# Kernel optimization log

Measured on AMD Instinct MI355X. Metric: run time of the kernel, lower is better.

## Reference

```python
import jax, jax.numpy as jnp
import numpy as np

MARGIN = 0.1
PERM_SEED = 42  # fixed stand-in for torch.randperm per row


def setup_inputs() -> dict:
    key = jax.random.key(0)
    k1, k2, k3 = jax.random.split(key, 3)
    n, d, f = 32768, 1000, 300
    inputs = jax.random.normal(k1, (n, f), dtype=jnp.float32)
    Y = jax.random.normal(k2, (d, f), dtype=jnp.float32)
    y_idxs = jax.random.randint(k3, (n,), 0, d)
    return {"inputs": inputs, "Y": Y, "y_idxs": y_idxs}


def reference(inputs, Y, y_idxs):
    # inputs: [n, f], Y: [d, f] class semantic embeddings, y_idxs: [n]
    n, d = inputs.shape[0], Y.shape[0]

    # All dot products at once: S[i, j] = Y[j] . inputs[i]
    S = inputs @ Y.T  # [n, d]

    # One random class permutation per row (torch.randperm(d) per sample)
    perm_keys = jax.random.split(jax.random.key(PERM_SEED), n)
    perms = jax.vmap(lambda k: jax.random.permutation(k, d))(perm_keys)  # [n, d]

    ap = S[jnp.arange(n), y_idxs]                 # [n]   anchor-positive dots
    an = jnp.take_along_axis(S, perms, axis=1)    # [n, d] anchor-negative dots in perm order

    valid = perms != y_idxs[:, None]              # skip j == y
    # early-break condition at each permutation slot
    cond = valid & ((ap[:, None] - an) > MARGIN)
    c = cond.astype(jnp.int32)
    excl_cum = jnp.cumsum(c, axis=1) - c          # exclusive cumsum of break events
    # include every valid slot up to AND including the first breaking slot
    include = valid & (excl_cum == 0)             # [n, d]

    # MarginRankingLoss with target=1: mean(max(0, margin + an - ap))
    per_pair = jnp.maximum(0.0, MARGIN + an - ap[:, None])
    total = jnp.sum(jnp.where(include, per_pair, 0.0))
    count = jnp.maximum(jnp.sum(include), 1).astype(jnp.float32)
    return total / count
```

## Files before the change

### kernel.cpp

```cpp
#include <hip/hip_runtime.h>
#include <stdint.h>

#define N_ROWS 32768
#define D_CLS  1000
#define D_PAD  1024
#define F_DIM  300
#define F_PAD  320
#define MARGIN 0.1f

#define BM     128
#define BN     128
#define BK     64
#define GTHR   512
#define LDTA   328
#define LDTB   72

#define M_PB   32
#define NTHR   512
#define NT_PW  8
#define MT_PB  2
#define LDA    328
#define SROW   34

#define NPART  32

typedef short short8 __attribute__((ext_vector_type(8)));
typedef float f32x4  __attribute__((ext_vector_type(4)));

__device__ __forceinline__ uint32_t rotl32(uint32_t x, int r) {
  return (x << r) | (x >> (32 - r));
}

__device__ __forceinline__ void threefry2x32(uint32_t k0, uint32_t k1,
                                             uint32_t x0, uint32_t x1,
                                             uint32_t& o0, uint32_t& o1) {
  uint32_t k2 = k0 ^ k1 ^ 0x1BD11BDAu;
  x0 += k0; x1 += k1;
#define TF_R(r) { x0 += x1; x1 = rotl32(x1, (r)); x1 ^= x0; }
  TF_R(13) TF_R(15) TF_R(26) TF_R(6)
  x0 += k1; x1 += k2 + 1u;
  TF_R(17) TF_R(29) TF_R(16) TF_R(24)
  x0 += k2; x1 += k0 + 2u;
  TF_R(13) TF_R(15) TF_R(26) TF_R(6)
  x0 += k0; x1 += k1 + 3u;
  TF_R(17) TF_R(29) TF_R(16) TF_R(24)
  x0 += k1; x1 += k2 + 4u;
  TF_R(13) TF_R(15) TF_R(26) TF_R(6)
  x0 += k2; x1 += k0 + 5u;
#undef TF_R
  o0 = x0; o1 = x1;
}

struct TFSched {
  uint32_t k0, k1, k2, k2p1, k0p2, k1p3, k2p4, k0p5;
};
__device__ __forceinline__ TFSched tf_make(uint32_t k0, uint32_t k1) {
  TFSched s;
  s.k0 = k0; s.k1 = k1;
  s.k2 = k0 ^ k1 ^ 0x1BD11BDAu;
  s.k2p1 = s.k2 + 1u; s.k0p2 = k0 + 2u; s.k1p3 = k1 + 3u;
  s.k2p4 = s.k2 + 4u; s.k0p5 = k0 + 5u;
  return s;
}
__device__ __forceinline__ uint32_t tf_hash(const TFSched& s, uint32_t c) {
  uint32_t x0 = s.k0, x1 = c + s.k1;
#define TFH(r) { x0 += x1; x1 = __builtin_amdgcn_alignbit(x1, x1, 32 - (r)); x1 ^= x0; }
  TFH(13) TFH(15) TFH(26) TFH(6)
  x0 += s.k1; x1 += s.k2p1;
  TFH(17) TFH(29) TFH(16) TFH(24)
  x0 += s.k2; x1 += s.k0p2;
  TFH(13) TFH(15) TFH(26) TFH(6)
  x0 += s.k0; x1 += s.k1p3;
  TFH(17) TFH(29) TFH(16) TFH(24)
  x0 += s.k1; x1 += s.k2p4;
  TFH(13) TFH(15) TFH(26) TFH(6)
  x0 += s.k2; x1 += s.k0p5;
#undef TFH
  return x0 ^ x1;
}

__device__ __forceinline__ uint16_t f2bf(float f) {
  uint32_t u = __builtin_bit_cast(uint32_t, f);
  return (uint16_t)((u + 0x7FFFu + ((u >> 16) & 1u)) >> 16);
}
__device__ __forceinline__ float bf2f(uint16_t v) {
  return __builtin_bit_cast(float, (uint32_t)v << 16);
}
__device__ __forceinline__ float bf2f_lo(uint32_t v) {
  return __builtin_bit_cast(float, v << 16);
}
__device__ __forceinline__ float bf2f_hi(uint32_t v) {
  return __builtin_bit_cast(float, v & 0xFFFF0000u);
}

__global__ void prep(const float* __restrict__ Y, uint16_t* __restrict__ Ybf,
                     uint32_t* __restrict__ subk) {
  int i = blockIdx.x * 256 + threadIdx.x;
  if (i < D_PAD * F_PAD) {
    int j = i / F_PAD;
    int k = i - j * F_PAD;
    float v = (j < D_CLS && k < F_DIM) ? Y[j * F_DIM + k] : 0.f;
    Ybf[i] = f2bf(v);
  }
  if (i < N_ROWS) {
    uint32_t r1, r2, s1, s2;
    threefry2x32(0u, 42u, 0u, (uint32_t)i, r1, r2);
    threefry2x32(r1, r2, 0u, 1u, s1, s2);
    subk[2 * i]     = s1;
    subk[2 * i + 1] = s2;
  }
}

template<int FUSED>
__launch_bounds__(GTHR, 1)
__global__ void gemm_core(const float* __restrict__ inputs,
                          const uint16_t* __restrict__ Ybf,
                          uint32_t* __restrict__ Spair,
                          uint32_t* __restrict__ keyP,
                          const uint32_t* __restrict__ subk,
                          const int* __restrict__ yidx,
                          float* __restrict__ rowSum,
                          int* __restrict__ rowCnt) {
  __shared__ __align__(16) uint16_t A_lds[BM * LDTA];
  __shared__ __align__(16) uint16_t B_lds[2][BN * LDTB];

  const int t    = threadIdx.x;
  const int wave = t >> 6;
  const int lane = t & 63;
  const int l15  = lane & 15;
  const int g    = lane >> 4;
  const int wm   = wave >> 1;
  const int wn   = wave & 1;
  const int r0   = blockIdx.x * BM;

  for (int i = t; i < BM * (F_DIM / 4); i += GTHR) {
    int r  = i / 75;
    int c4 = i - r * 75;
    float4 v = *(const float4*)(inputs + (size_t)(r0 + r) * F_DIM + c4 * 4);
    ushort4 o;
    o.x = f2bf(v.x); o.y = f2bf(v.y); o.z = f2bf(v.z); o.w = f2bf(v.w);
    *(ushort4*)&A_lds[r * LDTA + c4 * 4] = o;
  }
  for (int i = t; i < BM * 7; i += GTHR) {
    int r = i / 7, p = i - r * 7;
    *(ushort4*)&A_lds[r * LDTA + 300 + p * 4] = (ushort4){0, 0, 0, 0};
  }

  const int brow = t >> 3, bkof = t & 7;
  short8 bv[2];
  auto LOADB = [&](int tile) {
    const int c0 = (tile / 5) * BN;
    const int k0 = (tile % 5) * BK;
#pragma unroll
    for (int j = 0; j < 2; ++j)
      bv[j] = *(const short8*)(Ybf + (size_t)(c0 + j * 64 + brow) * F_PAD + k0 + bkof * 8);
  };
  auto WRITEB = [&](int buf) {
#pragma unroll
    for (int j = 0; j < 2; ++j)
      *(short8*)&B_lds[buf][(j * 64 + brow) * LDTB + bkof * 8] = bv[j];
  };

  f32x4 acc[2][4];
#pragma unroll
  for (int mt = 0; mt < 2; ++mt)
#pragma unroll
    for (int nt = 0; nt < 4; ++nt) acc[mt][nt] = (f32x4){0.f, 0.f, 0.f, 0.f};

  LOADB(0);
  __syncthreads();
  WRITEB(0);
  __syncthreads();

  const int NT = 8 * 5;
#pragma unroll 1
  for (int tile = 0; tile < NT; ++tile) {
    const int kt = tile % 5;
    if (tile < NT - 1) LOADB(tile + 1);

    if (FUSED && tile < 32) {
#pragma unroll
      for (int mm = 0; mm < 2; ++mm) {
        const int m = 2 * tile + mm;
        const size_t rpg = (size_t)(r0 >> 1) + m;
        const int rA = r0 + 2 * m;
        const TFSched sA = tf_make(subk[2 * rA],     subk[2 * rA + 1]);
        const TFSched sB = tf_make(subk[2 * rA + 2], subk[2 * rA + 3]);
#pragma unroll
        for (int half = 0; half < 2; ++half) {
          const uint32_t c = (uint32_t)(t + 512 * half);
          uint32_t kA = tf_hash(sA, c);
          uint32_t kB = tf_hash(sB, c);
          keyP[rpg * D_PAD + c] = (kA >> 16) | (kB & 0xFFFF0000u);
        }
      }
    }

    const uint16_t* Bc = B_lds[tile & 1];
#pragma unroll
    for (int ks = 0; ks < 2; ++ks) {
      short8 a[2], b[4];
#pragma unroll
      for (int mt = 0; mt < 2; ++mt)
        a[mt] = *(const short8*)&A_lds[(wm * 32 + mt * 16 + l15) * LDTA + kt * BK + ks * 32 + g * 8];
#pragma unroll
      for (int nt = 0; nt < 4; ++nt)
        b[nt] = *(const short8*)&Bc[(wn * 64 + nt * 16 + l15) * LDTB + ks * 32 + g * 8];
#pragma unroll
      for (int mt = 0; mt < 2; ++mt)
#pragma unroll
        for (int nt = 0; nt < 4; ++nt)
          acc[mt][nt] = __builtin_amdgcn_mfma_f32_16x16x32_bf16(a[mt], b[nt], acc[mt][nt], 0, 0, 0);
    }
    if (kt == 4) {
      const int c0 = (tile / 5) * BN;
#pragma unroll
      for (int mt = 0; mt < 2; ++mt)
#pragma unroll
        for (int nt = 0; nt < 4; ++nt) {
          const int col = c0 + wn * 64 + nt * 16 + l15;
#pragma unroll
          for (int p = 0; p < 2; ++p) {
            uint32_t lo = f2bf(acc[mt][nt][2 * p]);
            uint32_t hi = f2bf(acc[mt][nt][2 * p + 1]);
            size_t rp = (size_t)(r0 >> 1) + wm * 16 + mt * 8 + g * 2 + p;
            Spair[rp * D_PAD + col] = (hi << 16) | lo;
          }
          acc[mt][nt] = (f32x4){0.f, 0.f, 0.f, 0.f};
        }
    }
    if (tile < NT - 1) {
      WRITEB((tile + 1) & 1);
      __syncthreads();
    }
  }

  if (FUSED) {
    __syncthreads();
#pragma unroll 1
    for (int j = 0; j < 8; ++j) {
      const int rp_loc = wave * 8 + j;
      const size_t rpg = (size_t)(r0 >> 1) + rp_loc;
      const int rA = r0 + 2 * rp_loc;
      const int yA = yidx[rA], yB = yidx[rA + 1];
      const uint32_t* Sp = Spair + rpg * D_PAD;
      const uint32_t* Kp = keyP  + rpg * D_PAD;
      const float apA = bf2f_lo(Sp[yA]);
      const float apB = bf2f_hi(Sp[yB]);

      uint32_t an[16], kk[16];
#pragma unroll
      for (int q4 = 0; q4 < 4; ++q4) {
        uint4 v = *(const uint4*)(Sp + q4 * 256 + lane * 4);
        an[4 * q4 + 0] = v.x; an[4 * q4 + 1] = v.y;
        an[4 * q4 + 2] = v.z; an[4 * q4 + 3] = v.w;
        uint4 w = *(const uint4*)(Kp + q4 * 256 + lane * 4);
        kk[4 * q4 + 0] = w.x; kk[4 * q4 + 1] = w.y;
        kk[4 * q4 + 2] = w.z; kk[4 * q4 + 3] = w.w;
      }

      uint32_t mnA = 0xFFFFu, mnB = 0xFFFFu;
#pragma unroll
      for (int q = 0; q < 16; ++q) {
        const int c = (q >> 2) * 256 + lane * 4 + (q & 3);
        const uint32_t kA = kk[q] & 0xFFFFu, kB = kk[q] >> 16;
        const float anA = bf2f_lo(an[q]), anB = bf2f_hi(an[q]);
        if ((c < D_CLS) && (c != yA) && (apA - anA) > MARGIN) mnA = (kA < mnA) ? kA : mnA;
        if ((c < D_CLS) && (c != yB) && (apB - anB) > MARGIN) mnB = (kB < mnB) ? kB : mnB;
      }
#pragma unroll
      for (int off = 1; off < 64; off <<= 1) {
        uint32_t oA = __shfl_xor(mnA, off, 64);
        uint32_t oB = __shfl_xor(mnB, off, 64);
        mnA = (oA < mnA) ? oA : mnA;
        mnB = (oB < mnB) ? oB : mnB;
      }

      float smA = 0.f, smB = 0.f; int ctA = 0, ctB = 0;
#pragma unroll
      for (int q = 0; q < 16; ++q) {
        const int c = (q >> 2) * 256 + lane * 4 + (q & 3);
        const uint32_t kA = kk[q] & 0xFFFFu, kB = kk[q] >> 16;
        const float anA = bf2f_lo(an[q]), anB = bf2f_hi(an[q]);
        if ((c < D_CLS) && (c != yA) && kA < mnA) { smA += MARGIN + anA - apA; ctA += 1; }
        if ((c < D_CLS) && (c != yB) && kB < mnB) { smB += MARGIN + anB - apB; ctB += 1; }
      }
#pragma unroll
      for (int off = 1; off < 64; off <<= 1) {
        smA += __shfl_xor(smA, off, 64);
        smB += __shfl_xor(smB, off, 64);
        ctA += __shfl_xor(ctA, off, 64);
        ctB += __shfl_xor(ctB, off, 64);
      }
      if (lane == 0) {
        rowSum[rA]     = smA;  rowCnt[rA]     = ctA + (mnA != 0xFFFFu ? 1 : 0);
        rowSum[rA + 1] = smB;  rowCnt[rA + 1] = ctB + (mnB != 0xFFFFu ? 1 : 0);
      }
    }
  }
}

__launch_bounds__(256, 2)
__global__ void hash_loss(const uint32_t* __restrict__ Spair,
                          const uint32_t* __restrict__ subk,
                          const int* __restrict__ yidx,
                          float* __restrict__ rowSum,
                          int* __restrict__ rowCnt) {
  const int lane = threadIdx.x & 63;
  const int wave = threadIdx.x >> 6;
  const int rp   = blockIdx.x * 4 + wave;
  const int rA   = 2 * rp;
  const int rB   = 2 * rp + 1;

  const int yA = yidx[rA], yB = yidx[rB];
  const TFSched sA = tf_make(subk[2 * rA], subk[2 * rA + 1]);
  const TFSched sB = tf_make(subk[2 * rB], subk[2 * rB + 1]);

  const uint32_t* Sp = Spair + (size_t)rp * D_PAD;
  const float apA = bf2f_lo(Sp[yA]);
  const float apB = bf2f_hi(Sp[yB]);

  uint32_t an[16];
#pragma unroll
  for (int j = 0; j < 4; ++j) {
    uint4 v = *(const uint4*)(Sp + j * 256 + lane * 4);
    an[4 * j + 0] = v.x; an[4 * j + 1] = v.y;
    an[4 * j + 2] = v.z; an[4 * j + 3] = v.w;
  }

  uint32_t skAB[16];
  uint32_t pkA = 0xFFFFFFFFu, pkB = 0xFFFFFFFFu;
#pragma unroll
  for (int q = 0; q < 16; ++q) {
    const int c = (q >> 2) * 256 + lane * 4 + (q & 3);
    uint32_t kA = tf_hash(sA, (uint32_t)c);
    uint32_t kB = tf_hash(sB, (uint32_t)c);
    skAB[q] = (kA >> 16) | (kB & 0xFFFF0000u);
    float anA = bf2f_lo(an[q]);
    float anB = bf2f_hi(an[q]);
    if ((c < D_CLS) && (c != yA) && (apA - anA) > MARGIN) {
      pkA = (kA < pkA) ? kA : pkA;
    }
    if ((c < D_CLS) && (c != yB) && (apB - anB) > MARGIN) {
      pkB = (kB < pkB) ? kB : pkB;
    }
  }
#pragma unroll
  for (int off = 1; off < 64; off <<= 1) {
    uint32_t oA = __shfl_xor(pkA, off, 64);
    uint32_t oB = __shfl_xor(pkB, off, 64);
    pkA = (oA < pkA) ? oA : pkA;
    pkB = (oB < pkB) ? oB : pkB;
  }
  const uint32_t pA16 = pkA >> 16;
  const uint32_t pB16 = pkB >> 16;

  float smA = 0.f, smB = 0.f; int ctA = 0, ctB = 0;
#pragma unroll
  for (int q = 0; q < 16; ++q) {
    const int c = (q >> 2) * 256 + lane * 4 + (q & 3);
    float anA = bf2f_lo(an[q]);
    float anB = bf2f_hi(an[q]);
    if ((c < D_CLS) && (c != yA) && (skAB[q] & 0xFFFFu) < pA16) {
      smA += MARGIN + anA - apA; ctA += 1;
    }
    if ((c < D_CLS) && (c != yB) && (skAB[q] >> 16) < pB16) {
      smB += MARGIN + anB - apB; ctB += 1;
    }
  }
#pragma unroll
  for (int off = 1; off < 64; off <<= 1) {
    smA += __shfl_xor(smA, off, 64);
    smB += __shfl_xor(smB, off, 64);
    ctA += __shfl_xor(ctA, off, 64);
    ctB += __shfl_xor(ctB, off, 64);
  }
  if (lane == 0) {
    rowSum[rA] = smA;
    rowCnt[rA] = ctA + (pkA != 0xFFFFFFFFu ? 1 : 0);
    rowSum[rB] = smB;
    rowCnt[rB] = ctB + (pkB != 0xFFFFFFFFu ? 1 : 0);
  }
}

__launch_bounds__(NTHR, 4)
__global__ void triplet_fused(const float* __restrict__ inputs,
                              const uint16_t* __restrict__ Ybf,
                              const int* __restrict__ yidx,
                              float* __restrict__ rowSum,
                              int* __restrict__ rowCnt) {
  __shared__ __align__(16) uint16_t SH[D_PAD * SROW];
  __shared__ int      y_sh[M_PB];
  __shared__ uint32_t subk_sh[M_PB][2];

  const int t    = threadIdx.x;
  const int wave = t >> 6;
  const int lane = t & 63;
  const int l15  = lane & 15;
  const int g    = lane >> 4;
  const int row0 = blockIdx.x * M_PB;
  const int colbase = wave * (NT_PW * 16);

  if (t < M_PB) {
    y_sh[t] = yidx[row0 + t];
    uint32_t r1, r2, s1, s2;
    threefry2x32(0u, 42u, 0u, (uint32_t)(row0 + t), r1, r2);
    threefry2x32(r1, r2, 0u, 1u, s1, s2);
    subk_sh[t][0] = s1; subk_sh[t][1] = s2;
  }

  uint16_t* A_fl = SH;
  for (int i = t; i < M_PB * (F_DIM / 4); i += NTHR) {
    int r  = i / 75;
    int c4 = i - r * 75;
    float4 v = *(const float4*)(inputs + (size_t)(row0 + r) * F_DIM + c4 * 4);
    ushort4 o;
    o.x = f2bf(v.x); o.y = f2bf(v.y); o.z = f2bf(v.z); o.w = f2bf(v.w);
    *(ushort4*)&A_fl[r * LDA + c4 * 4] = o;
  }
  for (int i = t; i < M_PB * 5; i += NTHR) {
    int r = i / 5, p = i - r * 5;
    *(ushort4*)&A_fl[r * LDA + 300 + p * 4] = (ushort4){0, 0, 0, 0};
  }
  __syncthreads();

  f32x4 acc[MT_PB][NT_PW];
#pragma unroll
  for (int mt = 0; mt < MT_PB; ++mt)
#pragma unroll
    for (int nt = 0; nt < NT_PW; ++nt) acc[mt][nt] = (f32x4){0.f, 0.f, 0.f, 0.f};

  const uint16_t* gB[NT_PW];
#pragma unroll
  for (int nt = 0; nt < NT_PW; ++nt) {
    int j = colbase + nt * 16 + l15;
    gB[nt] = Ybf + (size_t)j * F_PAD + (g << 3);
  }
  const uint16_t* aBase = &A_fl[l15 * LDA + (g << 3)];

#pragma unroll 2
  for (int ks = 0; ks < F_PAD / 32; ++ks) {
    short8 b[NT_PW], a[MT_PB];
#pragma unroll
    for (int nt = 0; nt < NT_PW; ++nt)
      b[nt] = *(const short8*)(gB[nt] + ks * 32);
#pragma unroll
    for (int mt = 0; mt < MT_PB; ++mt)
      a[mt] = *(const short8*)(aBase + mt * 16 * LDA + ks * 32);
#pragma unroll
    for (int mt = 0; mt < MT_PB; ++mt)
#pragma unroll
      for (int nt = 0; nt < NT_PW; ++nt)
        acc[mt][nt] = __builtin_amdgcn_mfma_f32_16x16x32_bf16(a[mt], b[nt], acc[mt][nt], 0, 0, 0);
  }

  __syncthreads();

#pragma unroll
  for (int mt = 0; mt < MT_PB; ++mt)
#pragma unroll
    for (int nt = 0; nt < NT_PW; ++nt) {
      int col = colbase + nt * 16 + l15;
#pragma unroll
      for (int p = 0; p < 2; ++p) {
        uint32_t lo = f2bf(acc[mt][nt][2 * p]);
        uint32_t hi = f2bf(acc[mt][nt][2 * p + 1]);
        *(uint32_t*)&SH[col * SROW + mt * 16 + (g << 2) + 2 * p] = (hi << 16) | lo;
      }
    }
  __syncthreads();

#pragma unroll
  for (int pr = 0; pr < 2; ++pr) {
    const int rA = wave * 4 + pr * 2;
    const int rB = rA + 1;
    const int yA = y_sh[rA], yB = y_sh[rB];
    const uint32_t a1 = subk_sh[rA][0], a2 = subk_sh[rA][1];
    const uint32_t b1 = subk_sh[rB][0], b2 = subk_sh[rB][1];
    const float apA = bf2f(SH[yA * SROW + rA]);
    const float apB = bf2f(SH[yB * SROW + rB]);

    uint32_t skA[16], skB[16];
    uint32_t pkA = 0xFFFFFFFFu, pkB = 0xFFFFFFFFu;
#pragma unroll
    for (int q = 0; q < 16; ++q) {
      const int c = q * 64 + lane;
      uint32_t xA, yAo, xB, yBo;
      threefry2x32(a1, a2, 0u, (uint32_t)c, xA, yAo);
      threefry2x32(b1, b2, 0u, (uint32_t)c, xB, yBo);
      skA[q] = xA ^ yAo;
      skB[q] = xB ^ yBo;
      float anA = bf2f(SH[c * SROW + rA]);
      float anB = bf2f(SH[c * SROW + rB]);
      if ((c < D_CLS) && (c != yA) && (apA - anA) > MARGIN) {
        pkA = (skA[q] < pkA) ? skA[q] : pkA;
      }
      if ((c < D_CLS) && (c != yB) && (apB - anB) > MARGIN) {
        pkB = (skB[q] < pkB) ? skB[q] : pkB;
      }
    }
#pragma unroll
    for (int off = 1; off < 64; off <<= 1) {
      uint32_t oA = __shfl_xor(pkA, off, 64);
      uint32_t oB = __shfl_xor(pkB, off, 64);
      pkA = (oA < pkA) ? oA : pkA;
      pkB = (oB < pkB) ? oB : pkB;
    }
    float smA = 0.f, smB = 0.f; int ctA = 0, ctB = 0;
#pragma unroll
    for (int q = 0; q < 16; ++q) {
      const int c = q * 64 + lane;
      float anA = bf2f(SH[c * SROW + rA]);
      float anB = bf2f(SH[c * SROW + rB]);
      if ((c < D_CLS) && (c != yA) && skA[q] < pkA) { smA += MARGIN + anA - apA; ctA += 1; }
      if ((c < D_CLS) && (c != yB) && skB[q] < pkB) { smB += MARGIN + anB - apB; ctB += 1; }
    }
#pragma unroll
    for (int off = 1; off < 64; off <<= 1) {
      smA += __shfl_xor(smA, off, 64);
      smB += __shfl_xor(smB, off, 64);
      ctA += __shfl_xor(ctA, off, 64);
      ctB += __shfl_xor(ctB, off, 64);
    }
    if (lane == 0) {
      rowSum[row0 + rA] = smA;
      rowCnt[row0 + rA] = ctA + (pkA != 0xFFFFFFFFu ? 1 : 0);
      rowSum[row0 + rB] = smB;
      rowCnt[row0 + rB] = ctB + (pkB != 0xFFFFFFFFu ? 1 : 0);
    }
  }
}

__global__ void reduce_part(const float* __restrict__ rowSum,
                            const int* __restrict__ rowCnt,
                            float* __restrict__ pS, int* __restrict__ pC) {
  __shared__ float ss[4];
  __shared__ int   sc[4];
  const int base = blockIdx.x * (N_ROWS / NPART);
  float s = 0.f; int c = 0;
  for (int i = threadIdx.x; i < N_ROWS / NPART; i += 256) {
    s += rowSum[base + i];
    c += rowCnt[base + i];
  }
#pragma unroll
  for (int off = 32; off > 0; off >>= 1) {
    s += __shfl_down(s, (unsigned)off, 64);
    c += __shfl_down(c, (unsigned)off, 64);
  }
  int wid = threadIdx.x >> 6, lane = threadIdx.x & 63;
  if (lane == 0) { ss[wid] = s; sc[wid] = c; }
  __syncthreads();
  if (threadIdx.x == 0) {
    pS[blockIdx.x] = ss[0] + ss[1] + ss[2] + ss[3];
    pC[blockIdx.x] = sc[0] + sc[1] + sc[2] + sc[3];
  }
}

__global__ void reduce_final(const float* __restrict__ pS,
                             const int* __restrict__ pC,
                             float* __restrict__ out) {
  const int lane = threadIdx.x;
  float s = (lane < NPART) ? pS[lane] : 0.f;
  int   c = (lane < NPART) ? pC[lane] : 0;
#pragma unroll
  for (int off = 32; off > 0; off >>= 1) {
    s += __shfl_down(s, (unsigned)off, 64);
    c += __shfl_down(c, (unsigned)off, 64);
  }
  if (lane == 0) out[0] = s / (float)(c < 1 ? 1 : c);
}

extern "C" void kernel_launch(void* const* d_in, const int* in_sizes, int n_in,
                              void* d_out, int out_size, void* d_ws, size_t ws_size,
                              hipStream_t stream) {
  const float* inputs = (const float*)d_in[0];
  const float* Y      = (const float*)d_in[1];
  const int*   yidx   = (const int*)d_in[2];
  float* out = (float*)d_out;

  char* ws = (char*)d_ws;
  size_t off = 0;
  uint16_t* Ybf    = (uint16_t*)(ws + off); off += (size_t)D_PAD * F_PAD * 2;
  float*    rowSum = (float*)(ws + off);    off += (size_t)N_ROWS * 4;
  int*      rowCnt = (int*)(ws + off);      off += (size_t)N_ROWS * 4;
  uint32_t* subk   = (uint32_t*)(ws + off); off += (size_t)N_ROWS * 8;
  float*    pS     = (float*)(ws + off);    off += (size_t)NPART * 4;
  int*      pC     = (int*)(ws + off);      off += (size_t)NPART * 4;
  off = (off + 255) & ~(size_t)255;
  uint32_t* Spair  = (uint32_t*)(ws + off); off += (size_t)(N_ROWS / 2) * D_PAD * 4;
  const size_t need_mid = off;
  off = (off + 255) & ~(size_t)255;
  uint32_t* keyP   = (uint32_t*)(ws + off); off += (size_t)(N_ROWS / 2) * D_PAD * 4;
  const size_t need_full = off;

  hipLaunchKernelGGL(prep, dim3((D_PAD * F_PAD + 255) / 256), dim3(256),
                     0, stream, Y, Ybf, subk);
  if (ws_size >= need_full) {
    gemm_core<1><<<dim3(N_ROWS / BM), dim3(GTHR), 0, stream>>>(
        inputs, Ybf, Spair, keyP, subk, yidx, rowSum, rowCnt);
  } else if (ws_size >= need_mid) {
    gemm_core<0><<<dim3(N_ROWS / BM), dim3(GTHR), 0, stream>>>(
        inputs, Ybf, Spair, (uint32_t*)nullptr, subk, yidx, rowSum, rowCnt);
    hipLaunchKernelGGL(hash_loss, dim3(N_ROWS / 8), dim3(256),
                       0, stream, Spair, subk, yidx, rowSum, rowCnt);
  } else {
    hipLaunchKernelGGL(triplet_fused, dim3(N_ROWS / M_PB), dim3(NTHR),
                       0, stream, inputs, Ybf, yidx, rowSum, rowCnt);
  }
  hipLaunchKernelGGL(reduce_part, dim3(NPART), dim3(256), 0, stream,
                     rowSum, rowCnt, pS, pC);
  hipLaunchKernelGGL(reduce_final, dim3(1), dim3(64), 0, stream, pS, pC, out);
}
```

Before: 138.0 us.

## Warp-specialize GEMM with dedicated hash waves and split loss into separate kernel

The fused GEMM kernel is replaced by a 1024-thread block in which 8 waves do the MFMA GEMM while 8 extra waves compute the threefry permutation keys concurrently, writing them with vectorized 16-byte stores. The per-row loss evaluation moves out of the GEMM tail into a separate lightweight kernel. This is meant to overlap the hash ALU work with matrix math and to stop the loss tail from serializing inside the GEMM block. In exchange it adds a kernel launch, a re-read of Spair and keyP from memory, and a larger block that may reduce occupancy or register headroom.

After: 129.5 us. 1.07x faster.

```diff
diff --git a/kernel.cpp b/kernel.cpp
--- a/kernel.cpp
+++ b/kernel.cpp
@@ -12,6 +12,7 @@
 #define BN     128
 #define BK     64
 #define GTHR   512
+#define KGTHR  1024
 #define LDTA   328
 #define LDTB   72
 
@@ -111,16 +112,199 @@
   }
 }
 
-template<int FUSED>
+__launch_bounds__(KGTHR, 4)
+__global__ void gemm_kg(const float* __restrict__ inputs,
+                        const uint16_t* __restrict__ Ybf,
+                        uint32_t* __restrict__ Spair,
+                        uint32_t* __restrict__ keyP,
+                        const uint32_t* __restrict__ subk) {
+  __shared__ __align__(16) uint16_t A_lds[BM * LDTA];
+  __shared__ __align__(16) uint16_t B_lds[2][BN * LDTB];
+
+  const int t    = threadIdx.x;
+  const int wave = t >> 6;
+  const int lane = t & 63;
+  const int l15  = lane & 15;
+  const int g    = lane >> 4;
+  const bool isg = wave < 8;
+  const int wm   = wave >> 1;
+  const int wn   = wave & 1;
+  const int kw   = wave - 8;
+  const int r0   = blockIdx.x * BM;
+
+  for (int i = t; i < BM * (F_DIM / 4); i += KGTHR) {
+    int r  = i / 75;
+    int c4 = i - r * 75;
+    float4 v = *(const float4*)(inputs + (size_t)(r0 + r) * F_DIM + c4 * 4);
+    ushort4 o;
+    o.x = f2bf(v.x); o.y = f2bf(v.y); o.z = f2bf(v.z); o.w = f2bf(v.w);
+    *(ushort4*)&A_lds[r * LDTA + c4 * 4] = o;
+  }
+  for (int i = t; i < BM * 7; i += KGTHR) {
+    int r = i / 7, p = i - r * 7;
+    *(ushort4*)&A_lds[r * LDTA + 300 + p * 4] = (ushort4){0, 0, 0, 0};
+  }
+
+  const int brow = t >> 3, bkof = t & 7;
+  short8 bv[2];
+  auto LOADB = [&](int tile) {
+    const int c0 = (tile / 5) * BN;
+    const int k0 = (tile % 5) * BK;
+#pragma unroll
+    for (int j = 0; j < 2; ++j)
+      bv[j] = *(const short8*)(Ybf + (size_t)(c0 + j * 64 + brow) * F_PAD + k0 + bkof * 8);
+  };
+  auto WRITEB = [&](int buf) {
+#pragma unroll
+    for (int j = 0; j < 2; ++j)
+      *(short8*)&B_lds[buf][(j * 64 + brow) * LDTB + bkof * 8] = bv[j];
+  };
+
+  f32x4 acc[2][4];
+#pragma unroll
+  for (int mt = 0; mt < 2; ++mt)
+#pragma unroll
+    for (int nt = 0; nt < 4; ++nt) acc[mt][nt] = (f32x4){0.f, 0.f, 0.f, 0.f};
+
+  if (isg) LOADB(0);
+  __syncthreads();
+  if (isg) WRITEB(0);
+  __syncthreads();
+
+  const int NT = 8 * 5;
+#pragma unroll 1
+  for (int tile = 0; tile < NT; ++tile) {
+    if (isg) {
+      const int kt = tile % 5;
+      if (tile < NT - 1) LOADB(tile + 1);
+      const uint16_t* Bc = B_lds[tile & 1];
+#pragma unroll
+      for (int ks = 0; ks < 2; ++ks) {
+        short8 a[2], b[4];
+#pragma unroll
+        for (int mt = 0; mt < 2; ++mt)
+          a[mt] = *(const short8*)&A_lds[(wm * 32 + mt * 16 + l15) * LDTA + kt * BK + ks * 32 + g * 8];
+#pragma unroll
+        for (int nt = 0; nt < 4; ++nt)
+          b[nt] = *(const short8*)&Bc[(wn * 64 + nt * 16 + l15) * LDTB + ks * 32 + g * 8];
+#pragma unroll
+        for (int mt = 0; mt < 2; ++mt)
+#pragma unroll
+          for (int nt = 0; nt < 4; ++nt)
+            acc[mt][nt] = __builtin_amdgcn_mfma_f32_16x16x32_bf16(a[mt], b[nt], acc[mt][nt], 0, 0, 0);
+      }
+      if (kt == 4) {
+        const int c0 = (tile / 5) * BN;
+#pragma unroll
+        for (int mt = 0; mt < 2; ++mt)
+#pragma unroll
+          for (int nt = 0; nt < 4; ++nt) {
+            const int col = c0 + wn * 64 + nt * 16 + l15;
+#pragma unroll
+            for (int p = 0; p < 2; ++p) {
+              uint32_t lo = f2bf(acc[mt][nt][2 * p]);
+              uint32_t hi = f2bf(acc[mt][nt][2 * p + 1]);
+              size_t rp = (size_t)(r0 >> 1) + wm * 16 + mt * 8 + g * 2 + p;
+              Spair[rp * D_PAD + col] = (hi << 16) | lo;
+            }
+            acc[mt][nt] = (f32x4){0.f, 0.f, 0.f, 0.f};
+          }
+      }
+      if (tile < NT - 1) WRITEB((tile + 1) & 1);
+    } else if (tile < 32) {
+      const int rp_loc = kw * 8 + (tile >> 2);
+      const size_t rpg = (size_t)(r0 >> 1) + rp_loc;
+      const int rA = r0 + 2 * rp_loc;
+      const uint4 sk4 = *(const uint4*)(subk + 2 * rA);
+      const TFSched sA = tf_make(sk4.x, sk4.y);
+      const TFSched sB = tf_make(sk4.z, sk4.w);
+      const uint32_t c0 = (uint32_t)((tile & 3) * 256 + 4 * lane);
+      uint4 ov;
+      uint32_t o[4];
+#pragma unroll
+      for (int j = 0; j < 4; ++j) {
+        uint32_t kA = tf_hash(sA, c0 + (uint32_t)j);
+        uint32_t kB = tf_hash(sB, c0 + (uint32_t)j);
+        o[j] = (kA >> 16) | (kB & 0xFFFF0000u);
+      }
+      ov.x = o[0]; ov.y = o[1]; ov.z = o[2]; ov.w = o[3];
+      *(uint4*)(keyP + (rpg << 10) + c0) = ov;
+    }
+    if (tile < NT - 1) __syncthreads();
+  }
+}
+
+__launch_bounds__(256, 4)
+__global__ void loss_light(const uint32_t* __restrict__ Spair,
+                           const uint32_t* __restrict__ keyP,
+                           const int* __restrict__ yidx,
+                           float* __restrict__ rowSum,
+                           int* __restrict__ rowCnt) {
+  const int lane = threadIdx.x & 63;
+  const int wave = threadIdx.x >> 6;
+  const int rp   = blockIdx.x * 4 + wave;
+  const int rA   = 2 * rp;
+  const int rB   = rA + 1;
+  const int yA = yidx[rA], yB = yidx[rB];
+  const uint32_t* Sp = Spair + (size_t)rp * D_PAD;
+  const uint32_t* Kp = keyP  + (size_t)rp * D_PAD;
+  const float apA = bf2f_lo(Sp[yA]);
+  const float apB = bf2f_hi(Sp[yB]);
+
+  uint32_t an[16], kk[16];
+#pragma unroll
+  for (int q4 = 0; q4 < 4; ++q4) {
+    uint4 v = *(const uint4*)(Sp + q4 * 256 + lane * 4);
+    an[4 * q4 + 0] = v.x; an[4 * q4 + 1] = v.y;
+    an[4 * q4 + 2] = v.z; an[4 * q4 + 3] = v.w;
+    uint4 w = *(const uint4*)(Kp + q4 * 256 + lane * 4);
+    kk[4 * q4 + 0] = w.x; kk[4 * q4 + 1] = w.y;
+    kk[4 * q4 + 2] = w.z; kk[4 * q4 + 3] = w.w;
+  }
+
+  uint32_t mnA = 0xFFFFu, mnB = 0xFFFFu;
+#pragma unroll
+  for (int q = 0; q < 16; ++q) {
+    const int c = (q >> 2) * 256 + lane * 4 + (q & 3);
+    const uint32_t kA = kk[q] & 0xFFFFu, kB = kk[q] >> 16;
+    const float anA = bf2f_lo(an[q]), anB = bf2f_hi(an[q]);
+    if ((c < D_CLS) && (c != yA) && (apA - anA) > MARGIN) mnA = (kA < mnA) ? kA : mnA;
+    if ((c < D_CLS) && (c != yB) && (apB - anB) > MARGIN) mnB = (kB < mnB) ? kB : mnB;
+  }
+#pragma unroll
+  for (int off = 1; off < 64; off <<= 1) {
+    uint32_t oA = __shfl_xor(mnA, off, 64);
+    uint32_t oB = __shfl_xor(mnB, off, 64);
+    mnA = (oA < mnA) ? oA : mnA;
+    mnB = (oB < mnB) ? oB : mnB;
+  }
+
+  float smA = 0.f, smB = 0.f; int ctA = 0, ctB = 0;
+#pragma unroll
+  for (int q = 0; q < 16; ++q) {
+    const int c = (q >> 2) * 256 + lane * 4 + (q & 3);
+    const uint32_t kA = kk[q] & 0xFFFFu, kB = kk[q] >> 16;
+    const float anA = bf2f_lo(an[q]), anB = bf2f_hi(an[q]);
+    if ((c < D_CLS) && (c != yA) && kA < mnA) { smA += MARGIN + anA - apA; ctA += 1; }
+    if ((c < D_CLS) && (c != yB) && kB < mnB) { smB += MARGIN + anB - apB; ctB += 1; }
+  }
+#pragma unroll
+  for (int off = 1; off < 64; off <<= 1) {
+    smA += __shfl_xor(smA, off, 64);
+    smB += __shfl_xor(smB, off, 64);
+    ctA += __shfl_xor(ctA, off, 64);
+    ctB += __shfl_xor(ctB, off, 64);
+  }
+  if (lane == 0) {
+    rowSum[rA] = smA;  rowCnt[rA] = ctA + (mnA != 0xFFFFu ? 1 : 0);
+    rowSum[rB] = smB;  rowCnt[rB] = ctB + (mnB != 0xFFFFu ? 1 : 0);
+  }
+}
+
 __launch_bounds__(GTHR, 1)
-__global__ void gemm_core(const float* __restrict__ inputs,
-                          const uint16_t* __restrict__ Ybf,
-                          uint32_t* __restrict__ Spair,
-                          uint32_t* __restrict__ keyP,
-                          const uint32_t* __restrict__ subk,
-                          const int* __restrict__ yidx,
-                          float* __restrict__ rowSum,
-                          int* __restrict__ rowCnt) {
+__global__ void gemm_s(const float* __restrict__ inputs,
+                       const uint16_t* __restrict__ Ybf,
+                       uint32_t* __restrict__ Spair) {
   __shared__ __align__(16) uint16_t A_lds[BM * LDTA];
   __shared__ __align__(16) uint16_t B_lds[2][BN * LDTB];
 
@@ -177,25 +361,6 @@
   for (int tile = 0; tile < NT; ++tile) {
     const int kt = tile % 5;
     if (tile < NT - 1) LOADB(tile + 1);
-
-    if (FUSED && tile < 32) {
-#pragma unroll
-      for (int mm = 0; mm < 2; ++mm) {
-        const int m = 2 * tile + mm;
-        const size_t rpg = (size_t)(r0 >> 1) + m;
-        const int rA = r0 + 2 * m;
-        const TFSched sA = tf_make(subk[2 * rA],     subk[2 * rA + 1]);
-        const TFSched sB = tf_make(subk[2 * rA + 2], subk[2 * rA + 3]);
-#pragma unroll
-        for (int half = 0; half < 2; ++half) {
-          const uint32_t c = (uint32_t)(t + 512 * half);
-          uint32_t kA = tf_hash(sA, c);
-          uint32_t kB = tf_hash(sB, c);
-          keyP[rpg * D_PAD + c] = (kA >> 16) | (kB & 0xFFFF0000u);
-        }
-      }
-    }
-
     const uint16_t* Bc = B_lds[tile & 1];
 #pragma unroll
     for (int ks = 0; ks < 2; ++ks) {
@@ -232,70 +397,6 @@
     if (tile < NT - 1) {
       WRITEB((tile + 1) & 1);
       __syncthreads();
-    }
-  }
-
-  if (FUSED) {
-    __syncthreads();
-#pragma unroll 1
-    for (int j = 0; j < 8; ++j) {
-      const int rp_loc = wave * 8 + j;
-      const size_t rpg = (size_t)(r0 >> 1) + rp_loc;
-      const int rA = r0 + 2 * rp_loc;
-      const int yA = yidx[rA], yB = yidx[rA + 1];
-      const uint32_t* Sp = Spair + rpg * D_PAD;
-      const uint32_t* Kp = keyP  + rpg * D_PAD;
-      const float apA = bf2f_lo(Sp[yA]);
-      const float apB = bf2f_hi(Sp[yB]);
-
-      uint32_t an[16], kk[16];
-#pragma unroll
-      for (int q4 = 0; q4 < 4; ++q4) {
-        uint4 v = *(const uint4*)(Sp + q4 * 256 + lane * 4);
-        an[4 * q4 + 0] = v.x; an[4 * q4 + 1] = v.y;
-        an[4 * q4 + 2] = v.z; an[4 * q4 + 3] = v.w;
-        uint4 w = *(const uint4*)(Kp + q4 * 256 + lane * 4);
-        kk[4 * q4 + 0] = w.x; kk[4 * q4 + 1] = w.y;
-        kk[4 * q4 + 2] = w.z; kk[4 * q4 + 3] = w.w;
-      }
-
-      uint32_t mnA = 0xFFFFu, mnB = 0xFFFFu;
-#pragma unroll
-      for (int q = 0; q < 16; ++q) {
-        const int c = (q >> 2) * 256 + lane * 4 + (q & 3);
-        const uint32_t kA = kk[q] & 0xFFFFu, kB = kk[q] >> 16;
-        const float anA = bf2f_lo(an[q]), anB = bf2f_hi(an[q]);
-        if ((c < D_CLS) && (c != yA) && (apA - anA) > MARGIN) mnA = (kA < mnA) ? kA : mnA;
-        if ((c < D_CLS) && (c != yB) && (apB - anB) > MARGIN) mnB = (kB < mnB) ? kB : mnB;
-      }
-#pragma unroll
-      for (int off = 1; off < 64; off <<= 1) {
-        uint32_t oA = __shfl_xor(mnA, off, 64);
-        uint32_t oB = __shfl_xor(mnB, off, 64);
-        mnA = (oA < mnA) ? oA : mnA;
-        mnB = (oB < mnB) ? oB : mnB;
-      }
-
-      float smA = 0.f, smB = 0.f; int ctA = 0, ctB = 0;
-#pragma unroll
-      for (int q = 0; q < 16; ++q) {
-        const int c = (q >> 2) * 256 + lane * 4 + (q & 3);
-        const uint32_t kA = kk[q] & 0xFFFFu, kB = kk[q] >> 16;
-        const float anA = bf2f_lo(an[q]), anB = bf2f_hi(an[q]);
-        if ((c < D_CLS) && (c != yA) && kA < mnA) { smA += MARGIN + anA - apA; ctA += 1; }
-        if ((c < D_CLS) && (c != yB) && kB < mnB) { smB += MARGIN + anB - apB; ctB += 1; }
-      }
-#pragma unroll
-      for (int off = 1; off < 64; off <<= 1) {
-        smA += __shfl_xor(smA, off, 64);
-        smB += __shfl_xor(smB, off, 64);
-        ctA += __shfl_xor(ctA, off, 64);
-        ctB += __shfl_xor(ctB, off, 64);
-      }
-      if (lane == 0) {
-        rowSum[rA]     = smA;  rowCnt[rA]     = ctA + (mnA != 0xFFFFu ? 1 : 0);
-        rowSum[rA + 1] = smB;  rowCnt[rA + 1] = ctB + (mnB != 0xFFFFu ? 1 : 0);
-      }
     }
   }
 }
@@ -596,11 +697,13 @@
   hipLaunchKernelGGL(prep, dim3((D_PAD * F_PAD + 255) / 256), dim3(256),
                      0, stream, Y, Ybf, subk);
   if (ws_size >= need_full) {
-    gemm_core<1><<<dim3(N_ROWS / BM), dim3(GTHR), 0, stream>>>(
-        inputs, Ybf, Spair, keyP, subk, yidx, rowSum, rowCnt);
+    hipLaunchKernelGGL(gemm_kg, dim3(N_ROWS / BM), dim3(KGTHR),
+                       0, stream, inputs, Ybf, Spair, keyP, subk);
+    hipLaunchKernelGGL(loss_light, dim3(N_ROWS / 8), dim3(256),
+                       0, stream, Spair, keyP, yidx, rowSum, rowCnt);
   } else if (ws_size >= need_mid) {
-    gemm_core<0><<<dim3(N_ROWS / BM), dim3(GTHR), 0, stream>>>(
-        inputs, Ybf, Spair, (uint32_t*)nullptr, subk, yidx, rowSum, rowCnt);
+    hipLaunchKernelGGL(gemm_s, dim3(N_ROWS / BM), dim3(GTHR),
+                       0, stream, inputs, Ybf, Spair);
     hipLaunchKernelGGL(hash_loss, dim3(N_ROWS / 8), dim3(256),
                        0, stream, Spair, subk, yidx, rowSum, rowCnt);
   } else {
```
